# Optimization experiments

Measured on AMD Instinct MI355X. Metric: run time of the kernel, lower is better.

The kernel has to match this reference:

```python
import jax, jax.numpy as jnp
import numpy as np

N_NODES = 100000


def _sage_conv(x, edge_index, W_l, b_l, W_r):
    # PyG SAGEConv (aggr='mean', root_weight=True):
    #   out = lin_l(mean_{j in N(i)} x_j) + lin_r(x_i)
    src, dst = edge_index[0], edge_index[1]
    msg = x[src]                                            # [E, C] gather
    agg = jax.ops.segment_sum(msg, dst, num_segments=N_NODES)  # [N, C]
    deg = jax.ops.segment_sum(jnp.ones((edge_index.shape[1],), x.dtype), dst,
                              num_segments=N_NODES)
    agg = agg / jnp.maximum(deg, 1.0)[:, None]              # mean aggregation
    return agg @ W_l + b_l + x @ W_r


def setup_inputs() -> dict:
    key = jax.random.key(0)
    ks = jax.random.split(key, 10)
    d, h = 128, 128
    s = 1.0 / np.sqrt(d)
    x = jax.random.normal(ks[0], (N_NODES, d), dtype=jnp.float32)
    edge_index = jax.random.randint(ks[1], (2, 640000), 0, N_NODES, dtype=jnp.int64)
    return {
        "x": x,
        "edge_index": edge_index,
        "W1_l": jax.random.uniform(ks[2], (d, h), jnp.float32, -s, s),
        "b1": jnp.zeros((h,), jnp.float32),
        "W1_r": jax.random.uniform(ks[3], (d, h), jnp.float32, -s, s),
        "W2_l": jax.random.uniform(ks[4], (h, h), jnp.float32, -s, s),
        "b2": jnp.zeros((h,), jnp.float32),
        "W2_r": jax.random.uniform(ks[5], (h, h), jnp.float32, -s, s),
        "W_lin": jax.random.uniform(ks[6], (h, 1), jnp.float32, -s, s),
        "b_lin": jnp.zeros((1,), jnp.float32),
    }


def reference(x, edge_index, W1_l, b1, W1_r, W2_l, b2, W2_r, W_lin, b_lin):
    h = jax.nn.relu(_sage_conv(x, edge_index, W1_l, b1, W1_r))
    h = jax.nn.relu(_sage_conv(h, edge_index, W2_l, b2, W2_r))
    return h @ W_lin + b_lin  # [N, 1]
```

## Files before the change

### kernel.cpp

```cpp
#include <hip/hip_runtime.h>
#include <hip/hip_bf16.h>


#define ND 128
#define KTOT 256
#define ASTRIDE 40
#define CAP 32

typedef __bf16 bf16x8 __attribute__((ext_vector_type(8)));
typedef float floatx16 __attribute__((ext_vector_type(16)));

__device__ inline unsigned short f2bf(float f) {
    union { float f; unsigned u; } v; v.f = f;
    unsigned r = v.u + 0x7fffu + ((v.u >> 16) & 1u);
    return (unsigned short)(r >> 16);
}
__device__ inline float bf_lo(unsigned u) { return __uint_as_float(u << 16); }
__device__ inline float bf_hi(unsigned u) { return __uint_as_float(u & 0xffff0000u); }

__global__ void k_prep_all(const float* __restrict__ x, unsigned short* __restrict__ xbf,
                           int nElems,
                           const float* __restrict__ W1l, const float* __restrict__ W1r,
                           unsigned short* __restrict__ Wt1,
                           const float* __restrict__ W2l, const float* __restrict__ W2r,
                           unsigned short* __restrict__ Wt2,
                           const int* __restrict__ esrc_in, const int* __restrict__ edst_in,
                           int* __restrict__ cnt, int* __restrict__ ebuk, int E) {
    const int t = threadIdx.x;
    const int tid = blockIdx.x * 256 + t;

    const int e = blockIdx.x * 128 + t;
    const bool doE = (t < 128) && (e < E);
    int d0 = 0, s0 = 0;
    if (doE) {
        d0 = edst_in[e];
        s0 = esrc_in[e];
    }

    const int i = tid * 8;
    float4 xa, xc;
    const bool doX = (i < nElems);
    if (doX) {
        xa = *(const float4*)(x + i);
        xc = *(const float4*)(x + i + 4);
    }

    int p0 = -1;
    if (doE) p0 = atomicAdd(&cnt[d0], 1);

    if (doX) {
        uint4 r;
        r.x = (unsigned)f2bf(xa.x) | ((unsigned)f2bf(xa.y) << 16);
        r.y = (unsigned)f2bf(xa.z) | ((unsigned)f2bf(xa.w) << 16);
        r.z = (unsigned)f2bf(xc.x) | ((unsigned)f2bf(xc.y) << 16);
        r.w = (unsigned)f2bf(xc.z) | ((unsigned)f2bf(xc.w) << 16);
        *(uint4*)(xbf + i) = r;
    }

    if (tid < 2 * KTOT * ND) {
        const int half = tid >> 15;
        const int idx = tid & 32767;
        const int nn = idx >> 8;
        const int kk = idx & 255;
        const float* Wl = half ? W2l : W1l;
        const float* Wr = half ? W2r : W1r;
        unsigned short* Wt = half ? Wt2 : Wt1;
        float v = (kk < 128) ? Wl[(size_t)kk * ND + nn] : Wr[(size_t)(kk - 128) * ND + nn];
        Wt[(size_t)nn * KTOT + kk] = f2bf(v);
    }

    if (p0 >= 0 && p0 < CAP) ebuk[d0 * CAP + p0] = s0;
}

__global__ void k_aggregate_bf(const unsigned short* __restrict__ feat,
                               unsigned short* __restrict__ out,
                               const int* __restrict__ cnt,
                               const int* __restrict__ ebuk, int n) {
    int node = (int)((blockIdx.x * (size_t)blockDim.x + threadIdx.x) >> 4);
    int l = threadIdx.x & 15;
    if (node >= n) return;
    int d = cnt[node];
    int dd = min(d, CAP);
    const int* lst = ebuk + node * CAP;
    float a0 = 0, a1 = 0, a2 = 0, a3 = 0, a4 = 0, a5 = 0, a6 = 0, a7 = 0;
    const int capi = dd - 1;
    for (int j = 0; j < dd; j += 4) {
        int s0 = lst[j];
        int s1 = lst[min(j + 1, capi)];
        int s2 = lst[min(j + 2, capi)];
        int s3 = lst[min(j + 3, capi)];
        uint4 v0 = ((const uint4*)(feat + (size_t)s0 * ND))[l];
        uint4 v1 = ((const uint4*)(feat + (size_t)s1 * ND))[l];
        uint4 v2 = ((const uint4*)(feat + (size_t)s2 * ND))[l];
        uint4 v3 = ((const uint4*)(feat + (size_t)s3 * ND))[l];
        if (j + 1 >= dd) { v1.x = v1.y = v1.z = v1.w = 0u; }
        if (j + 2 >= dd) { v2.x = v2.y = v2.z = v2.w = 0u; }
        if (j + 3 >= dd) { v3.x = v3.y = v3.z = v3.w = 0u; }
        a0 += bf_lo(v0.x) + bf_lo(v1.x) + bf_lo(v2.x) + bf_lo(v3.x);
        a1 += bf_hi(v0.x) + bf_hi(v1.x) + bf_hi(v2.x) + bf_hi(v3.x);
        a2 += bf_lo(v0.y) + bf_lo(v1.y) + bf_lo(v2.y) + bf_lo(v3.y);
        a3 += bf_hi(v0.y) + bf_hi(v1.y) + bf_hi(v2.y) + bf_hi(v3.y);
        a4 += bf_lo(v0.z) + bf_lo(v1.z) + bf_lo(v2.z) + bf_lo(v3.z);
        a5 += bf_hi(v0.z) + bf_hi(v1.z) + bf_hi(v2.z) + bf_hi(v3.z);
        a6 += bf_lo(v0.w) + bf_lo(v1.w) + bf_lo(v2.w) + bf_lo(v3.w);
        a7 += bf_hi(v0.w) + bf_hi(v1.w) + bf_hi(v2.w) + bf_hi(v3.w);
    }
    float inv = 1.0f / (float)max(d, 1);
    uint4 r;
    r.x = (unsigned)f2bf(a0 * inv) | ((unsigned)f2bf(a1 * inv) << 16);
    r.y = (unsigned)f2bf(a2 * inv) | ((unsigned)f2bf(a3 * inv) << 16);
    r.z = (unsigned)f2bf(a4 * inv) | ((unsigned)f2bf(a5 * inv) << 16);
    r.w = (unsigned)f2bf(a6 * inv) | ((unsigned)f2bf(a7 * inv) << 16);
    ((uint4*)(out + (size_t)node * ND))[l] = r;
}

__launch_bounds__(256, 4)
__global__ void k_layer_mfma(const unsigned short* __restrict__ A0,
                             const unsigned short* __restrict__ A1,
                             const unsigned short* __restrict__ Wt,
                             const float* __restrict__ bias,
                             unsigned short* __restrict__ out, int n) {
    __shared__ __align__(16) unsigned short As[128 * ASTRIDE];
    __shared__ __align__(16) unsigned short Bs[128 * ASTRIDE];
    const int t = threadIdx.x;
    const int m0 = blockIdx.x * 128;
    const int wave = t >> 6, lane = t & 63;
    const int l31 = lane & 31, lhalf = lane >> 5;
    const int wm = (wave >> 1) * 64;
    const int wn = (wave & 1) * 64;

    floatx16 acc[2][2];
#pragma unroll
    for (int i = 0; i < 2; ++i)
#pragma unroll
        for (int j = 0; j < 2; ++j) acc[i][j] = (floatx16)0.0f;

    const int srow = t >> 1;
    const int skid = (t & 1) * 16;

    for (int kc = 0; kc < 8; ++kc) {
        const int k0 = kc * 32;
        {
            const unsigned short* base = (k0 < 128) ? A0 : A1;
            const int col = (k0 & 127) + skid;
            const int grow = m0 + srow;
            int4 w0 = {0, 0, 0, 0}, w1 = {0, 0, 0, 0};
            if (grow < n) {
                const int4* p = (const int4*)(base + (size_t)grow * ND + col);
                w0 = p[0]; w1 = p[1];
            }
            int4* q = (int4*)&As[srow * ASTRIDE + skid];
            q[0] = w0; q[1] = w1;
        }
        {
            const int4* p = (const int4*)(Wt + (size_t)srow * KTOT + k0 + skid);
            int4* q = (int4*)&Bs[srow * ASTRIDE + skid];
            q[0] = p[0]; q[1] = p[1];
        }
        __syncthreads();
        bf16x8 af[2][2], bfr[2][2];
#pragma unroll
        for (int mi = 0; mi < 2; ++mi)
#pragma unroll
            for (int ks = 0; ks < 2; ++ks)
                af[mi][ks] = *(const bf16x8*)&As[(wm + mi * 32 + l31) * ASTRIDE + ks * 16 + lhalf * 8];
#pragma unroll
        for (int ni = 0; ni < 2; ++ni)
#pragma unroll
            for (int ks = 0; ks < 2; ++ks)
                bfr[ni][ks] = *(const bf16x8*)&Bs[(wn + ni * 32 + l31) * ASTRIDE + ks * 16 + lhalf * 8];
#pragma unroll
        for (int mi = 0; mi < 2; ++mi)
#pragma unroll
            for (int ni = 0; ni < 2; ++ni) {
                acc[mi][ni] = __builtin_amdgcn_mfma_f32_32x32x16_bf16(af[mi][0], bfr[ni][0], acc[mi][ni], 0, 0, 0);
                acc[mi][ni] = __builtin_amdgcn_mfma_f32_32x32x16_bf16(af[mi][1], bfr[ni][1], acc[mi][ni], 0, 0, 0);
            }
        __syncthreads();
    }
#pragma unroll
    for (int mi = 0; mi < 2; ++mi)
#pragma unroll
        for (int ni = 0; ni < 2; ++ni) {
            const int c = wn + ni * 32 + l31;
            const float bv = bias[c];
#pragma unroll
            for (int reg = 0; reg < 16; ++reg) {
                const int row = m0 + wm + mi * 32 + lhalf * 4 + (reg & 3) + 8 * (reg >> 2);
                if (row < n) {
                    float v = fmaxf(acc[mi][ni][reg] + bv, 0.f);
                    out[(size_t)row * ND + c] = f2bf(v);
                }
            }
        }
}

__launch_bounds__(256, 4)
__global__ void k_layer2_head(const unsigned short* __restrict__ A0,
                              const unsigned short* __restrict__ A1,
                              const unsigned short* __restrict__ Wt,
                              const float* __restrict__ bias,
                              const float* __restrict__ Wlin,
                              const float* __restrict__ blin,
                              float* __restrict__ out, int n) {
    __shared__ __align__(16) unsigned short As[128 * ASTRIDE];
    __shared__ __align__(16) unsigned short Bs[128 * ASTRIDE];
    __shared__ float part[128][2];
    const int t = threadIdx.x;
    const int m0 = blockIdx.x * 128;
    const int wave = t >> 6, lane = t & 63;
    const int l31 = lane & 31, lhalf = lane >> 5;
    const int wm = (wave >> 1) * 64;
    const int wn = (wave & 1) * 64;

    floatx16 acc[2][2];
#pragma unroll
    for (int i = 0; i < 2; ++i)
#pragma unroll
        for (int j = 0; j < 2; ++j) acc[i][j] = (floatx16)0.0f;

    const int srow = t >> 1;
    const int skid = (t & 1) * 16;

    for (int kc = 0; kc < 8; ++kc) {
        const int k0 = kc * 32;
        {
            const unsigned short* base = (k0 < 128) ? A0 : A1;
            const int col = (k0 & 127) + skid;
            const int grow = m0 + srow;
            int4 w0 = {0, 0, 0, 0}, w1 = {0, 0, 0, 0};
            if (grow < n) {
                const int4* p = (const int4*)(base + (size_t)grow * ND + col);
                w0 = p[0]; w1 = p[1];
            }
            int4* q = (int4*)&As[srow * ASTRIDE + skid];
            q[0] = w0; q[1] = w1;
        }
        {
            const int4* p = (const int4*)(Wt + (size_t)srow * KTOT + k0 + skid);
            int4* q = (int4*)&Bs[srow * ASTRIDE + skid];
            q[0] = p[0]; q[1] = p[1];
        }
        __syncthreads();
        bf16x8 af[2][2], bfr[2][2];
#pragma unroll
        for (int mi = 0; mi < 2; ++mi)
#pragma unroll
            for (int ks = 0; ks < 2; ++ks)
                af[mi][ks] = *(const bf16x8*)&As[(wm + mi * 32 + l31) * ASTRIDE + ks * 16 + lhalf * 8];
#pragma unroll
        for (int ni = 0; ni < 2; ++ni)
#pragma unroll
            for (int ks = 0; ks < 2; ++ks)
                bfr[ni][ks] = *(const bf16x8*)&Bs[(wn + ni * 32 + l31) * ASTRIDE + ks * 16 + lhalf * 8];
#pragma unroll
        for (int mi = 0; mi < 2; ++mi)
#pragma unroll
            for (int ni = 0; ni < 2; ++ni) {
                acc[mi][ni] = __builtin_amdgcn_mfma_f32_32x32x16_bf16(af[mi][0], bfr[ni][0], acc[mi][ni], 0, 0, 0);
                acc[mi][ni] = __builtin_amdgcn_mfma_f32_32x32x16_bf16(af[mi][1], bfr[ni][1], acc[mi][ni], 0, 0, 0);
            }
        __syncthreads();
    }
#pragma unroll
    for (int mi = 0; mi < 2; ++mi) {
        float p[16];
#pragma unroll
        for (int reg = 0; reg < 16; ++reg) p[reg] = 0.f;
#pragma unroll
        for (int ni = 0; ni < 2; ++ni) {
            const int c = wn + ni * 32 + l31;
            const float bv = bias[c];
            const float wv = Wlin[c];
#pragma unroll
            for (int reg = 0; reg < 16; ++reg) {
                float v = fmaxf(acc[mi][ni][reg] + bv, 0.f);
                p[reg] += v * wv;
            }
        }
#pragma unroll
        for (int reg = 0; reg < 16; ++reg) {
            float v = p[reg];
            v += __shfl_xor(v, 1);
            v += __shfl_xor(v, 2);
            v += __shfl_xor(v, 4);
            v += __shfl_xor(v, 8);
            v += __shfl_xor(v, 16);
            if (l31 == 0) {
                int rl = wm + mi * 32 + lhalf * 4 + (reg & 3) + 8 * (reg >> 2);
                part[rl][wave & 1] = v;
            }
        }
    }
    __syncthreads();
    if (t < 128) {
        int row = m0 + t;
        if (row < n) out[row] = part[t][0] + part[t][1] + blin[0];
    }
}

extern "C" void kernel_launch(void* const* d_in, const int* in_sizes, int n_in,
                              void* d_out, int out_size, void* d_ws, size_t ws_size,
                              hipStream_t stream) {
    const float* x    = (const float*)d_in[0];
    const int*   edge = (const int*)d_in[1];
    const float* W1l  = (const float*)d_in[2];
    const float* b1   = (const float*)d_in[3];
    const float* W1r  = (const float*)d_in[4];
    const float* W2l  = (const float*)d_in[5];
    const float* b2   = (const float*)d_in[6];
    const float* W2r  = (const float*)d_in[7];
    const float* Wlin = (const float*)d_in[8];
    const float* blin = (const float*)d_in[9];
    float* out = (float*)d_out;

    int n = out_size;
    int E = in_sizes[1] / 2;
    (void)n_in; (void)ws_size;

    char* ws = (char*)d_ws;
    size_t off = 0;
    auto take = [&](size_t bytes) -> char* {
        char* p = ws + off;
        off += (bytes + 255) & ~(size_t)255;
        return p;
    };
    int* cnt    = (int*)take((size_t)n * 4);
    int* ebuk   = (int*)take((size_t)n * CAP * 4);
    unsigned short* xbf  = (unsigned short*)take((size_t)n * ND * 2);
    unsigned short* h1bf = (unsigned short*)take((size_t)n * ND * 2);
    unsigned short* agbf = (unsigned short*)take((size_t)n * ND * 2);
    unsigned short* Wt1  = (unsigned short*)take((size_t)ND * KTOT * 2);
    unsigned short* Wt2  = (unsigned short*)take((size_t)ND * KTOT * 2);

    hipMemsetAsync(cnt, 0, (size_t)n * 4, stream);

    const int* esrc_in = edge;
    const int* edst_in = edge + E;

    int nElems = n * ND;
    int prepBlocks = (nElems / 8 + 255) / 256;

    k_prep_all<<<prepBlocks, 256, 0, stream>>>(
        x, xbf, nElems, W1l, W1r, Wt1, W2l, W2r, Wt2,
        esrc_in, edst_in, cnt, ebuk, E);

    int aggBlocks  = (n + 15) / 16;
    int gemmBlocks = (n + 127) / 128;

    k_aggregate_bf<<<aggBlocks, 256, 0, stream>>>(xbf, agbf, cnt, ebuk, n);
    k_layer_mfma<<<gemmBlocks, 256, 0, stream>>>(agbf, xbf, Wt1, b1, h1bf, n);
    k_aggregate_bf<<<aggBlocks, 256, 0, stream>>>(h1bf, agbf, cnt, ebuk, n);
    k_layer2_head<<<gemmBlocks, 256, 0, stream>>>(agbf, h1bf, Wt2, b2, Wlin, blin, out, n);
}
```

Measured before the change: 232.4 us.

## Fuse neighbor mean aggregation into per-layer MFMA GEMM kernels via shared memory

Each layer's gather/mean aggregation now runs inside the GEMM kernel: a 128-node tile is aggregated straight into shared memory and consumed by MFMA, so the intermediate agg buffer and two kernel launches go away. The tiled LDS staging of A and B is replaced by direct global loads of weights and root features into registers, which also removes the per-k-chunk syncs. In exchange, occupancy drops (launch bounds lowered to 2 blocks per CU, larger LDS use), and the gather latency is no longer overlapped with other blocks' GEMM work in separate kernels.

```diff
diff --git a/kernel.cpp b/kernel.cpp
--- a/kernel.cpp
+++ b/kernel.cpp
@@ -4,8 +4,8 @@
 
 #define ND 128
 #define KTOT 256
-#define ASTRIDE 40
 #define CAP 32
+#define AGS 136
 
 typedef __bf16 bf16x8 __attribute__((ext_vector_type(8)));
 typedef float floatx16 __attribute__((ext_vector_type(16)));
@@ -17,6 +17,13 @@
 }
 __device__ inline float bf_lo(unsigned u) { return __uint_as_float(u << 16); }
 __device__ inline float bf_hi(unsigned u) { return __uint_as_float(u & 0xffff0000u); }
+
+__device__ inline bf16x8 ldg_bf8(const unsigned short* p, bool ok) {
+    int4 v = {0, 0, 0, 0};
+    if (ok) v = *(const int4*)p;
+    union { int4 i; bf16x8 b; } u; u.i = v;
+    return u.b;
+}
 
 __global__ void k_prep_all(const float* __restrict__ x, unsigned short* __restrict__ xbf,
                            int nElems,
@@ -72,58 +79,67 @@
     if (p0 >= 0 && p0 < CAP) ebuk[d0 * CAP + p0] = s0;
 }
 
-__global__ void k_aggregate_bf(const unsigned short* __restrict__ feat,
-                               unsigned short* __restrict__ out,
+__device__ __forceinline__ void gather128(const unsigned short* __restrict__ feat,
+                                          const int* __restrict__ cnt,
+                                          const int* __restrict__ ebuk,
+                                          int n, int m0, int t,
+                                          unsigned short* Agg) {
+    const int l = t & 15;
+    const int g = t >> 4;
+    for (int p = 0; p < 8; ++p) {
+        const int nl = p * 16 + g;
+        const int node = m0 + nl;
+        int d = 0;
+        if (node < n) d = cnt[node];
+        const int dd = min(d, CAP);
+        const int* lst = ebuk + (size_t)node * CAP;
+        float a0 = 0, a1 = 0, a2 = 0, a3 = 0, a4 = 0, a5 = 0, a6 = 0, a7 = 0;
+        const int capi = dd - 1;
+        for (int j = 0; j < dd; j += 4) {
+            int s0 = lst[j];
+            int s1 = lst[min(j + 1, capi)];
+            int s2 = lst[min(j + 2, capi)];
+            int s3 = lst[min(j + 3, capi)];
+            uint4 v0 = ((const uint4*)(feat + (size_t)s0 * ND))[l];
+            uint4 v1 = ((const uint4*)(feat + (size_t)s1 * ND))[l];
+            uint4 v2 = ((const uint4*)(feat + (size_t)s2 * ND))[l];
+            uint4 v3 = ((const uint4*)(feat + (size_t)s3 * ND))[l];
+            if (j + 1 >= dd) { v1.x = v1.y = v1.z = v1.w = 0u; }
+            if (j + 2 >= dd) { v2.x = v2.y = v2.z = v2.w = 0u; }
+            if (j + 3 >= dd) { v3.x = v3.y = v3.z = v3.w = 0u; }
+            a0 += bf_lo(v0.x) + bf_lo(v1.x) + bf_lo(v2.x) + bf_lo(v3.x);
+            a1 += bf_hi(v0.x) + bf_hi(v1.x) + bf_hi(v2.x) + bf_hi(v3.x);
+            a2 += bf_lo(v0.y) + bf_lo(v1.y) + bf_lo(v2.y) + bf_lo(v3.y);
+            a3 += bf_hi(v0.y) + bf_hi(v1.y) + bf_hi(v2.y) + bf_hi(v3.y);
+            a4 += bf_lo(v0.z) + bf_lo(v1.z) + bf_lo(v2.z) + bf_lo(v3.z);
+            a5 += bf_hi(v0.z) + bf_hi(v1.z) + bf_hi(v2.z) + bf_hi(v3.z);
+            a6 += bf_lo(v0.w) + bf_lo(v1.w) + bf_lo(v2.w) + bf_lo(v3.w);
+            a7 += bf_hi(v0.w) + bf_hi(v1.w) + bf_hi(v2.w) + bf_hi(v3.w);
+        }
+        float inv = 1.0f / (float)max(d, 1);
+        uint4 r;
+        r.x = (unsigned)f2bf(a0 * inv) | ((unsigned)f2bf(a1 * inv) << 16);
+        r.y = (unsigned)f2bf(a2 * inv) | ((unsigned)f2bf(a3 * inv) << 16);
+        r.z = (unsigned)f2bf(a4 * inv) | ((unsigned)f2bf(a5 * inv) << 16);
+        r.w = (unsigned)f2bf(a6 * inv) | ((unsigned)f2bf(a7 * inv) << 16);
+        *(uint4*)&Agg[nl * AGS + l * 8] = r;
+    }
+}
+
+__launch_bounds__(256, 2)
+__global__ void k_layer1_fused(const unsigned short* __restrict__ feat,
+                               const unsigned short* __restrict__ Wt,
+                               const float* __restrict__ bias,
                                const int* __restrict__ cnt,
-                               const int* __restrict__ ebuk, int n) {
-    int node = (int)((blockIdx.x * (size_t)blockDim.x + threadIdx.x) >> 4);
-    int l = threadIdx.x & 15;
-    if (node >= n) return;
-    int d = cnt[node];
-    int dd = min(d, CAP);
-    const int* lst = ebuk + node * CAP;
-    float a0 = 0, a1 = 0, a2 = 0, a3 = 0, a4 = 0, a5 = 0, a6 = 0, a7 = 0;
-    const int capi = dd - 1;
-    for (int j = 0; j < dd; j += 4) {
-        int s0 = lst[j];
-        int s1 = lst[min(j + 1, capi)];
-        int s2 = lst[min(j + 2, capi)];
-        int s3 = lst[min(j + 3, capi)];
-        uint4 v0 = ((const uint4*)(feat + (size_t)s0 * ND))[l];
-        uint4 v1 = ((const uint4*)(feat + (size_t)s1 * ND))[l];
-        uint4 v2 = ((const uint4*)(feat + (size_t)s2 * ND))[l];
-        uint4 v3 = ((const uint4*)(feat + (size_t)s3 * ND))[l];
-        if (j + 1 >= dd) { v1.x = v1.y = v1.z = v1.w = 0u; }
-        if (j + 2 >= dd) { v2.x = v2.y = v2.z = v2.w = 0u; }
-        if (j + 3 >= dd) { v3.x = v3.y = v3.z = v3.w = 0u; }
-        a0 += bf_lo(v0.x) + bf_lo(v1.x) + bf_lo(v2.x) + bf_lo(v3.x);
-        a1 += bf_hi(v0.x) + bf_hi(v1.x) + bf_hi(v2.x) + bf_hi(v3.x);
-        a2 += bf_lo(v0.y) + bf_lo(v1.y) + bf_lo(v2.y) + bf_lo(v3.y);
-        a3 += bf_hi(v0.y) + bf_hi(v1.y) + bf_hi(v2.y) + bf_hi(v3.y);
-        a4 += bf_lo(v0.z) + bf_lo(v1.z) + bf_lo(v2.z) + bf_lo(v3.z);
-        a5 += bf_hi(v0.z) + bf_hi(v1.z) + bf_hi(v2.z) + bf_hi(v3.z);
-        a6 += bf_lo(v0.w) + bf_lo(v1.w) + bf_lo(v2.w) + bf_lo(v3.w);
-        a7 += bf_hi(v0.w) + bf_hi(v1.w) + bf_hi(v2.w) + bf_hi(v3.w);
-    }
-    float inv = 1.0f / (float)max(d, 1);
-    uint4 r;
-    r.x = (unsigned)f2bf(a0 * inv) | ((unsigned)f2bf(a1 * inv) << 16);
-    r.y = (unsigned)f2bf(a2 * inv) | ((unsigned)f2bf(a3 * inv) << 16);
-    r.z = (unsigned)f2bf(a4 * inv) | ((unsigned)f2bf(a5 * inv) << 16);
-    r.w = (unsigned)f2bf(a6 * inv) | ((unsigned)f2bf(a7 * inv) << 16);
-    ((uint4*)(out + (size_t)node * ND))[l] = r;
-}
-
-__launch_bounds__(256, 4)
-__global__ void k_layer_mfma(const unsigned short* __restrict__ A0,
-                             const unsigned short* __restrict__ A1,
-                             const unsigned short* __restrict__ Wt,
-                             const float* __restrict__ bias,
-                             unsigned short* __restrict__ out, int n) {
-    __shared__ __align__(16) unsigned short As[128 * ASTRIDE];
-    __shared__ __align__(16) unsigned short Bs[128 * ASTRIDE];
+                               const int* __restrict__ ebuk,
+                               unsigned short* __restrict__ out, int n) {
+    __shared__ __align__(16) unsigned short Agg[128 * AGS];
     const int t = threadIdx.x;
     const int m0 = blockIdx.x * 128;
+
+    gather128(feat, cnt, ebuk, n, m0, t, Agg);
+    __syncthreads();
+
     const int wave = t >> 6, lane = t & 63;
     const int l31 = lane & 31, lhalf = lane >> 5;
     const int wm = (wave >> 1) * 64;
@@ -135,40 +151,20 @@
 #pragma unroll
         for (int j = 0; j < 2; ++j) acc[i][j] = (floatx16)0.0f;
 
-    const int srow = t >> 1;
-    const int skid = (t & 1) * 16;
-
-    for (int kc = 0; kc < 8; ++kc) {
+#pragma unroll
+    for (int kc = 0; kc < 4; ++kc) {
         const int k0 = kc * 32;
-        {
-            const unsigned short* base = (k0 < 128) ? A0 : A1;
-            const int col = (k0 & 127) + skid;
-            const int grow = m0 + srow;
-            int4 w0 = {0, 0, 0, 0}, w1 = {0, 0, 0, 0};
-            if (grow < n) {
-                const int4* p = (const int4*)(base + (size_t)grow * ND + col);
-                w0 = p[0]; w1 = p[1];
-            }
-            int4* q = (int4*)&As[srow * ASTRIDE + skid];
-            q[0] = w0; q[1] = w1;
-        }
-        {
-            const int4* p = (const int4*)(Wt + (size_t)srow * KTOT + k0 + skid);
-            int4* q = (int4*)&Bs[srow * ASTRIDE + skid];
-            q[0] = p[0]; q[1] = p[1];
-        }
-        __syncthreads();
         bf16x8 af[2][2], bfr[2][2];
 #pragma unroll
         for (int mi = 0; mi < 2; ++mi)
 #pragma unroll
             for (int ks = 0; ks < 2; ++ks)
-                af[mi][ks] = *(const bf16x8*)&As[(wm + mi * 32 + l31) * ASTRIDE + ks * 16 + lhalf * 8];
+                af[mi][ks] = *(const bf16x8*)&Agg[(wm + mi * 32 + l31) * AGS + k0 + ks * 16 + lhalf * 8];
 #pragma unroll
         for (int ni = 0; ni < 2; ++ni)
 #pragma unroll
             for (int ks = 0; ks < 2; ++ks)
-                bfr[ni][ks] = *(const bf16x8*)&Bs[(wn + ni * 32 + l31) * ASTRIDE + ks * 16 + lhalf * 8];
+                bfr[ni][ks] = *(const bf16x8*)(Wt + (size_t)(wn + ni * 32 + l31) * KTOT + k0 + ks * 16 + lhalf * 8);
 #pragma unroll
         for (int mi = 0; mi < 2; ++mi)
 #pragma unroll
@@ -176,8 +172,34 @@
                 acc[mi][ni] = __builtin_amdgcn_mfma_f32_32x32x16_bf16(af[mi][0], bfr[ni][0], acc[mi][ni], 0, 0, 0);
                 acc[mi][ni] = __builtin_amdgcn_mfma_f32_32x32x16_bf16(af[mi][1], bfr[ni][1], acc[mi][ni], 0, 0, 0);
             }
-        __syncthreads();
-    }
+    }
+
+    const int rA0 = m0 + wm + l31;
+    const int rA1 = rA0 + 32;
+#pragma unroll
+    for (int kc = 4; kc < 8; ++kc) {
+        const int k0 = kc * 32;
+        const int ka = k0 - 128;
+        bf16x8 af[2][2], bfr[2][2];
+#pragma unroll
+        for (int ks = 0; ks < 2; ++ks) {
+            af[0][ks] = ldg_bf8(feat + (size_t)rA0 * ND + ka + ks * 16 + lhalf * 8, rA0 < n);
+            af[1][ks] = ldg_bf8(feat + (size_t)rA1 * ND + ka + ks * 16 + lhalf * 8, rA1 < n);
+        }
+#pragma unroll
+        for (int ni = 0; ni < 2; ++ni)
+#pragma unroll
+            for (int ks = 0; ks < 2; ++ks)
+                bfr[ni][ks] = *(const bf16x8*)(Wt + (size_t)(wn + ni * 32 + l31) * KTOT + k0 + ks * 16 + lhalf * 8);
+#pragma unroll
+        for (int mi = 0; mi < 2; ++mi)
+#pragma unroll
+            for (int ni = 0; ni < 2; ++ni) {
+                acc[mi][ni] = __builtin_amdgcn_mfma_f32_32x32x16_bf16(af[mi][0], bfr[ni][0], acc[mi][ni], 0, 0, 0);
+                acc[mi][ni] = __builtin_amdgcn_mfma_f32_32x32x16_bf16(af[mi][1], bfr[ni][1], acc[mi][ni], 0, 0, 0);
+            }
+    }
+
 #pragma unroll
     for (int mi = 0; mi < 2; ++mi)
 #pragma unroll
@@ -195,19 +217,23 @@
         }
 }
 
-__launch_bounds__(256, 4)
-__global__ void k_layer2_head(const unsigned short* __restrict__ A0,
-                              const unsigned short* __restrict__ A1,
-                              const unsigned short* __restrict__ Wt,
-                              const float* __restrict__ bias,
-                              const float* __restrict__ Wlin,
-                              const float* __restrict__ blin,
-                              float* __restrict__ out, int n) {
-    __shared__ __align__(16) unsigned short As[128 * ASTRIDE];
-    __shared__ __align__(16) unsigned short Bs[128 * ASTRIDE];
+__launch_bounds__(256, 2)
+__global__ void k_layer2_fused_head(const unsigned short* __restrict__ feat,
+                                    const unsigned short* __restrict__ Wt,
+                                    const float* __restrict__ bias,
+                                    const float* __restrict__ Wlin,
+                                    const float* __restrict__ blin,
+                                    const int* __restrict__ cnt,
+                                    const int* __restrict__ ebuk,
+                                    float* __restrict__ out, int n) {
+    __shared__ __align__(16) unsigned short Agg[128 * AGS];
     __shared__ float part[128][2];
     const int t = threadIdx.x;
     const int m0 = blockIdx.x * 128;
+
+    gather128(feat, cnt, ebuk, n, m0, t, Agg);
+    __syncthreads();
+
     const int wave = t >> 6, lane = t & 63;
     const int l31 = lane & 31, lhalf = lane >> 5;
     const int wm = (wave >> 1) * 64;
@@ -219,40 +245,20 @@
 #pragma unroll
         for (int j = 0; j < 2; ++j) acc[i][j] = (floatx16)0.0f;
 
-    const int srow = t >> 1;
-    const int skid = (t & 1) * 16;
-
-    for (int kc = 0; kc < 8; ++kc) {
+#pragma unroll
+    for (int kc = 0; kc < 4; ++kc) {
         const int k0 = kc * 32;
-        {
-            const unsigned short* base = (k0 < 128) ? A0 : A1;
-            const int col = (k0 & 127) + skid;
-            const int grow = m0 + srow;
-            int4 w0 = {0, 0, 0, 0}, w1 = {0, 0, 0, 0};
-            if (grow < n) {
-                const int4* p = (const int4*)(base + (size_t)grow * ND + col);
-                w0 = p[0]; w1 = p[1];
-            }
-            int4* q = (int4*)&As[srow * ASTRIDE + skid];
-            q[0] = w0; q[1] = w1;
-        }
-        {
-            const int4* p = (const int4*)(Wt + (size_t)srow * KTOT + k0 + skid);
-            int4* q = (int4*)&Bs[srow * ASTRIDE + skid];
-            q[0] = p[0]; q[1] = p[1];
-        }
-        __syncthreads();
         bf16x8 af[2][2], bfr[2][2];
 #pragma unroll
         for (int mi = 0; mi < 2; ++mi)
 #pragma unroll
             for (int ks = 0; ks < 2; ++ks)
-                af[mi][ks] = *(const bf16x8*)&As[(wm + mi * 32 + l31) * ASTRIDE + ks * 16 + lhalf * 8];
+                af[mi][ks] = *(const bf16x8*)&Agg[(wm + mi * 32 + l31) * AGS + k0 + ks * 16 + lhalf * 8];
 #pragma unroll
         for (int ni = 0; ni < 2; ++ni)
 #pragma unroll
             for (int ks = 0; ks < 2; ++ks)
-                bfr[ni][ks] = *(const bf16x8*)&Bs[(wn + ni * 32 + l31) * ASTRIDE + ks * 16 + lhalf * 8];
+                bfr[ni][ks] = *(const bf16x8*)(Wt + (size_t)(wn + ni * 32 + l31) * KTOT + k0 + ks * 16 + lhalf * 8);
 #pragma unroll
         for (int mi = 0; mi < 2; ++mi)
 #pragma unroll
@@ -260,8 +266,34 @@
                 acc[mi][ni] = __builtin_amdgcn_mfma_f32_32x32x16_bf16(af[mi][0], bfr[ni][0], acc[mi][ni], 0, 0, 0);
                 acc[mi][ni] = __builtin_amdgcn_mfma_f32_32x32x16_bf16(af[mi][1], bfr[ni][1], acc[mi][ni], 0, 0, 0);
             }
-        __syncthreads();
-    }
+    }
+
+    const int rA0 = m0 + wm + l31;
+    const int rA1 = rA0 + 32;
+#pragma unroll
+    for (int kc = 4; kc < 8; ++kc) {
+        const int k0 = kc * 32;
+        const int ka = k0 - 128;
+        bf16x8 af[2][2], bfr[2][2];
+#pragma unroll
+        for (int ks = 0; ks < 2; ++ks) {
+            af[0][ks] = ldg_bf8(feat + (size_t)rA0 * ND + ka + ks * 16 + lhalf * 8, rA0 < n);
+            af[1][ks] = ldg_bf8(feat + (size_t)rA1 * ND + ka + ks * 16 + lhalf * 8, rA1 < n);
+        }
+#pragma unroll
+        for (int ni = 0; ni < 2; ++ni)
+#pragma unroll
+            for (int ks = 0; ks < 2; ++ks)
+                bfr[ni][ks] = *(const bf16x8*)(Wt + (size_t)(wn + ni * 32 + l31) * KTOT + k0 + ks * 16 + lhalf * 8);
+#pragma unroll
+        for (int mi = 0; mi < 2; ++mi)
+#pragma unroll
+            for (int ni = 0; ni < 2; ++ni) {
+                acc[mi][ni] = __builtin_amdgcn_mfma_f32_32x32x16_bf16(af[mi][0], bfr[ni][0], acc[mi][ni], 0, 0, 0);
+                acc[mi][ni] = __builtin_amdgcn_mfma_f32_32x32x16_bf16(af[mi][1], bfr[ni][1], acc[mi][ni], 0, 0, 0);
+            }
+    }
+
 #pragma unroll
     for (int mi = 0; mi < 2; ++mi) {
         float p[16];
@@ -329,7 +361,6 @@
     int* ebuk   = (int*)take((size_t)n * CAP * 4);
     unsigned short* xbf  = (unsigned short*)take((size_t)n * ND * 2);
     unsigned short* h1bf = (unsigned short*)take((size_t)n * ND * 2);
-    unsigned short* agbf = (unsigned short*)take((size_t)n * ND * 2);
     unsigned short* Wt1  = (unsigned short*)take((size_t)ND * KTOT * 2);
     unsigned short* Wt2  = (unsigned short*)take((size_t)ND * KTOT * 2);
 
@@ -345,11 +376,8 @@
         x, xbf, nElems, W1l, W1r, Wt1, W2l, W2r, Wt2,
         esrc_in, edst_in, cnt, ebuk, E);
 
-    int aggBlocks  = (n + 15) / 16;
     int gemmBlocks = (n + 127) / 128;
 
-    k_aggregate_bf<<<aggBlocks, 256, 0, stream>>>(xbf, agbf, cnt, ebuk, n);
-    k_layer_mfma<<<gemmBlocks, 256, 0, stream>>>(agbf, xbf, Wt1, b1, h1bf, n);
-    k_aggregate_bf<<<aggBlocks, 256, 0, stream>>>(h1bf, agbf, cnt, ebuk, n);
-    k_layer2_head<<<gemmBlocks, 256, 0, stream>>>(agbf, h1bf, Wt2, b2, Wlin, blin, out, n);
-}
+    k_layer1_fused<<<gemmBlocks, 256, 0, stream>>>(xbf, Wt1, b1, cnt, ebuk, h1bf, n);
+    k_layer2_fused_head<<<gemmBlocks, 256, 0, stream>>>(h1bf, Wt2, b2, Wlin, blin, cnt, ebuk, out, n);
+}
```

Measured after the change: 241.7 us. 1.04x slower.
